# Kernel optimization log

Measured on AMD Instinct MI355X. Metric: run time of the kernel, lower is better.

Reference implementation:

```python
import jax, jax.numpy as jnp
import numpy as np

DIM = 4096
N_HEADS = 32
N_KV_HEADS = 8
HEAD_DIM = DIM // N_HEADS  # 128
SEQ = 2048
ROPE_THETA = 500000.0


def precompute_freqs_cis(head_dim, end, theta=ROPE_THETA):
    freq = 1.0 / theta ** (jnp.arange(0, head_dim, 2, dtype=jnp.float32) / head_dim)
    t = jnp.arange(end, dtype=jnp.float32)
    freqs = jnp.outer(t, freq)  # [S, D/2]
    return jnp.cos(freqs), jnp.sin(freqs)


def apply_rope(x, cos, sin):
    # x: [S, H, D]; cos/sin: [S, D/2]; interleaved even/odd rotation
    x_even = x[:, :, 0::2]
    x_odd = x[:, :, 1::2]
    c = cos[:, None, :]
    s = sin[:, None, :]
    rot_even = x_even * c - x_odd * s
    rot_odd = x_even * s + x_odd * c
    # re-interleave: stack on last axis then flatten -> [e0,o0,e1,o1,...]
    return jnp.stack([rot_even, rot_odd], axis=-1).reshape(x.shape)


def setup_inputs() -> dict:
    key = jax.random.key(0)
    ks = jax.random.split(key, 5)
    scale = 1.0 / np.sqrt(DIM)
    x = jax.random.normal(ks[0], (SEQ, DIM), dtype=jnp.float32)
    wq = jax.random.normal(ks[1], (DIM, DIM), dtype=jnp.float32) * scale
    wk = jax.random.normal(ks[2], (N_KV_HEADS * HEAD_DIM, DIM), dtype=jnp.float32) * scale
    wv = jax.random.normal(ks[3], (N_KV_HEADS * HEAD_DIM, DIM), dtype=jnp.float32) * scale
    wo = jax.random.normal(ks[4], (DIM, DIM), dtype=jnp.float32) * scale
    return {"x": x, "wq": wq, "wk": wk, "wv": wv, "wo": wo}


def reference(x, wq, wk, wv, wo):
    seq_len = x.shape[0]
    Q = (x @ wq.T).reshape(seq_len, N_HEADS, HEAD_DIM)
    K = (x @ wk.T).reshape(seq_len, N_KV_HEADS, HEAD_DIM)
    V = (x @ wv.T).reshape(seq_len, N_KV_HEADS, HEAD_DIM)
    cos, sin = precompute_freqs_cis(HEAD_DIM, seq_len)
    Q = apply_rope(Q, cos, sin)
    K = apply_rope(K, cos, sin)
    rep = N_HEADS // N_KV_HEADS
    K_rep = jnp.repeat(K, rep, axis=1)  # [S, H, D]
    V_rep = jnp.repeat(V, rep, axis=1)
    scores = jnp.einsum('qhd,khd->hqk', Q, K_rep) / np.sqrt(HEAD_DIM).astype(np.float32)
    causal = jnp.triu(jnp.ones((seq_len, seq_len), dtype=bool), k=1)
    scores = jnp.where(causal[None, :, :], -jnp.inf, scores)
    probs = jax.nn.softmax(scores.astype(jnp.float32), axis=-1).astype(Q.dtype)
    out = jnp.einsum('hqk,khd->qhd', probs, V_rep).reshape(seq_len, N_HEADS * HEAD_DIM)
    return out @ wo.T
```

## Files before the change

kernel.cpp:

```cpp
#include <hip/hip_runtime.h>
#include <stdint.h>
#include <math.h>

#define DIM 4096
#define NH 32
#define NKV 8
#define HD 128
#define SEQ 2048
#define KVDIM (NKV * HD)
#define QKVDIM (DIM + 2 * KVDIM)

typedef __bf16 bf16x8 __attribute__((ext_vector_type(8)));
typedef float floatx4 __attribute__((ext_vector_type(4)));
typedef uint16_t u16x8 __attribute__((ext_vector_type(8)));

#define AS1C(p) ((const __attribute__((address_space(1))) void*)(p))
#define AS3(p)  ((__attribute__((address_space(3))) void*)(p))

__device__ __forceinline__ float b2f(uint16_t u) {
    union { uint32_t i; float f; } v; v.i = ((uint32_t)u) << 16; return v.f;
}
__device__ __forceinline__ uint16_t f2b(float f) {
    union { float f; uint32_t i; } v; v.f = f;
    uint32_t r = v.i + 0x7fffu + ((v.i >> 16) & 1u);
    return (uint16_t)(r >> 16);
}

__device__ __forceinline__ u16x8 ldchunk(const void* p, bool isf32, size_t e) {
    if (isf32) {
        const float* fp = (const float*)p + e;
        u16x8 r;
#pragma unroll
        for (int j = 0; j < 8; ++j) r[j] = f2b(fp[j]);
        return r;
    }
    return *(const u16x8*)((const uint16_t*)p + e);
}

__global__ void detect_k(const uint16_t* __restrict__ x, int* __restrict__ flag) {
    __shared__ int cnt;
    if (threadIdx.x == 0) cnt = 0;
    __syncthreads();
    int bad = 0;
    for (int i = threadIdx.x; i < 4096; i += 256) {
        float v = b2f(x[i]);
        if (!(fabsf(v) < 1e6f)) bad++;
    }
    atomicAdd(&cnt, bad);
    __syncthreads();
    if (threadIdx.x == 0) *flag = (cnt > 256) ? 1 : 0;
}

__global__ __launch_bounds__(256) void conv_k(const void* __restrict__ src,
                                              uint16_t* __restrict__ dst,
                                              size_t n,
                                              const int* __restrict__ flagp) {
    const int f = *flagp;
    size_t i = ((size_t)blockIdx.x * blockDim.x + threadIdx.x) * 8;
    const size_t stride = (size_t)gridDim.x * blockDim.x * 8;
    if (f) {
        for (; i < n; i += stride) {
            const float* s = (const float*)src + i;
            u16x8 r;
#pragma unroll
            for (int j = 0; j < 8; ++j) r[j] = f2b(s[j]);
            *(u16x8*)(dst + i) = r;
        }
    } else {
        for (; i < n; i += stride)
            *(u16x8*)(dst + i) = *(const u16x8*)((const uint16_t*)src + i);
    }
}

__global__ __launch_bounds__(256) void gemm_nt(const void* __restrict__ A,
                                               const void* __restrict__ B,
                                               void* __restrict__ C,
                                               int K, int ldc,
                                               const int* __restrict__ flagp,
                                               int a_dyn, int b_dyn, int out_dyn,
                                               int out_trans) {
    __shared__ uint16_t As[128 * 64];
    __shared__ uint16_t Bs[128 * 64];
    const int f = *flagp;
    const bool af32 = a_dyn && f, bf32 = b_dyn && f, of32 = out_dyn && f;
    const int tid = threadIdx.x;
    const int wave = tid >> 6, lane = tid & 63;
    const int wh = wave >> 1, ww = wave & 1;
    const int quad = lane >> 4, l16 = lane & 15;
    const int m0 = blockIdx.x * 128;
    const int n0 = blockIdx.y * 128;

    floatx4 acc[4][4] = {};

    for (int k0 = 0; k0 < K; k0 += 64) {
        __syncthreads();
#pragma unroll
        for (int it = 0; it < 4; ++it) {
            int id = tid + it * 256;
            int row = id >> 3, slot = id & 7;
            int c8 = ((slot ^ (row & 7)) << 3);
            u16x8 va = ldchunk(A, af32, (size_t)(m0 + row) * K + k0 + c8);
            *(u16x8*)(As + row * 64 + slot * 8) = va;
            u16x8 vb = ldchunk(B, bf32, (size_t)(n0 + row) * K + k0 + c8);
            *(u16x8*)(Bs + row * 64 + slot * 8) = vb;
        }
        __syncthreads();
#pragma unroll
        for (int ks = 0; ks < 2; ++ks) {
            bf16x8 af[4], bf[4];
#pragma unroll
            for (int mi = 0; mi < 4; ++mi) {
                int r = wh * 64 + mi * 16 + l16;
                int slot = (ks * 4 + quad) ^ (r & 7);
                af[mi] = *(const bf16x8*)(As + r * 64 + slot * 8);
            }
#pragma unroll
            for (int ni = 0; ni < 4; ++ni) {
                int r = ww * 64 + ni * 16 + l16;
                int slot = (ks * 4 + quad) ^ (r & 7);
                bf[ni] = *(const bf16x8*)(Bs + r * 64 + slot * 8);
            }
#pragma unroll
            for (int mi = 0; mi < 4; ++mi)
#pragma unroll
                for (int ni = 0; ni < 4; ++ni)
                    acc[mi][ni] = __builtin_amdgcn_mfma_f32_16x16x32_bf16(
                        af[mi], bf[ni], acc[mi][ni], 0, 0, 0);
        }
    }
#pragma unroll
    for (int mi = 0; mi < 4; ++mi) {
#pragma unroll
        for (int ni = 0; ni < 4; ++ni) {
            int row = m0 + wh * 64 + mi * 16 + quad * 4;
            int col = n0 + ww * 64 + ni * 16 + l16;
            if (out_trans) {
                uint64_t pack = 0;
#pragma unroll
                for (int i = 0; i < 4; ++i)
                    pack |= (uint64_t)f2b(acc[mi][ni][i]) << (16 * i);
                *(uint64_t*)((uint16_t*)C + (size_t)col * ldc + row) = pack;
            } else if (of32) {
#pragma unroll
                for (int i = 0; i < 4; ++i)
                    ((float*)C)[(size_t)(row + i) * ldc + col] = acc[mi][ni][i];
            } else {
#pragma unroll
                for (int i = 0; i < 4; ++i)
                    ((uint16_t*)C)[(size_t)(row + i) * ldc + col] = f2b(acc[mi][ni][i]);
            }
        }
    }
}

__global__ __launch_bounds__(256) void gemm_bf(const uint16_t* __restrict__ A,
                                               const uint16_t* __restrict__ B,
                                               void* __restrict__ C,
                                               int K, int ldc,
                                               const int* __restrict__ flagp,
                                               int out_mode) {
    __shared__ uint16_t As[128 * 64];
    __shared__ uint16_t Bs[128 * 64];
    const bool of32 = (out_mode == 1) && (*flagp);
    const int tid = threadIdx.x;
    const int wave = tid >> 6, lane = tid & 63;
    const int wh = wave >> 1, ww = wave & 1;
    const int quad = lane >> 4, l16 = lane & 15;

    int nwg = gridDim.x * gridDim.y;
    int id = blockIdx.y * gridDim.x + blockIdx.x;
    if ((nwg & 7) == 0) {
        int cpx = nwg >> 3;
        id = (id & 7) * cpx + (id >> 3);
    }
    const int m0 = (id % gridDim.x) * 128;
    const int n0 = (id / gridDim.x) * 128;

    floatx4 acc[4][4] = {};

    for (int k0 = 0; k0 < K; k0 += 64) {
        __syncthreads();
#pragma unroll
        for (int it = 0; it < 4; ++it) {
            int idc = tid + it * 256;
            int row = idc >> 3, slot = idc & 7;
            int c8 = ((slot ^ (row & 7)) << 3);
            __builtin_amdgcn_global_load_lds(
                AS1C(A + (size_t)(m0 + row) * K + k0 + c8),
                AS3(As + (size_t)(it * 256 + wave * 64) * 8), 16, 0, 0);
            __builtin_amdgcn_global_load_lds(
                AS1C(B + (size_t)(n0 + row) * K + k0 + c8),
                AS3(Bs + (size_t)(it * 256 + wave * 64) * 8), 16, 0, 0);
        }
        __syncthreads();
#pragma unroll
        for (int ks = 0; ks < 2; ++ks) {
            bf16x8 af[4], bf[4];
#pragma unroll
            for (int mi = 0; mi < 4; ++mi) {
                int r = wh * 64 + mi * 16 + l16;
                int slot = (ks * 4 + quad) ^ (r & 7);
                af[mi] = *(const bf16x8*)(As + r * 64 + slot * 8);
            }
#pragma unroll
            for (int ni = 0; ni < 4; ++ni) {
                int r = ww * 64 + ni * 16 + l16;
                int slot = (ks * 4 + quad) ^ (r & 7);
                bf[ni] = *(const bf16x8*)(Bs + r * 64 + slot * 8);
            }
#pragma unroll
            for (int mi = 0; mi < 4; ++mi)
#pragma unroll
                for (int ni = 0; ni < 4; ++ni)
                    acc[mi][ni] = __builtin_amdgcn_mfma_f32_16x16x32_bf16(
                        af[mi], bf[ni], acc[mi][ni], 0, 0, 0);
        }
    }
#pragma unroll
    for (int mi = 0; mi < 4; ++mi) {
#pragma unroll
        for (int ni = 0; ni < 4; ++ni) {
            int row = m0 + wh * 64 + mi * 16 + quad * 4;
            int col = n0 + ww * 64 + ni * 16 + l16;
            if (of32) {
#pragma unroll
                for (int i = 0; i < 4; ++i)
                    ((float*)C)[(size_t)(row + i) * ldc + col] = acc[mi][ni][i];
            } else {
#pragma unroll
                for (int i = 0; i < 4; ++i)
                    ((uint16_t*)C)[(size_t)(row + i) * ldc + col] = f2b(acc[mi][ni][i]);
            }
        }
    }
}

__global__ __launch_bounds__(256) void gemm_qkv(const uint16_t* __restrict__ A,
                                                const uint16_t* __restrict__ W,
                                                uint16_t* __restrict__ Qo,
                                                uint16_t* __restrict__ Ko,
                                                uint16_t* __restrict__ VoT) {
    __shared__ uint16_t As[128 * 64];
    __shared__ uint16_t Bs[128 * 64];
    const int tid = threadIdx.x;
    const int wave = tid >> 6, lane = tid & 63;
    const int wh = wave >> 1, ww = wave & 1;
    const int quad = lane >> 4, l16 = lane & 15;

    int nwg = gridDim.x * gridDim.y;
    int id = blockIdx.y * gridDim.x + blockIdx.x;
    int cpx = nwg >> 3;
    id = (id & 7) * cpx + (id >> 3);
    const int m0 = (id % gridDim.x) * 128;
    const int n0 = (id / gridDim.x) * 128;
    const int K = DIM;

    floatx4 acc[4][4] = {};

    for (int k0 = 0; k0 < K; k0 += 64) {
        __syncthreads();
#pragma unroll
        for (int it = 0; it < 4; ++it) {
            int idc = tid + it * 256;
            int row = idc >> 3, slot = idc & 7;
            int c8 = ((slot ^ (row & 7)) << 3);
            __builtin_amdgcn_global_load_lds(
                AS1C(A + (size_t)(m0 + row) * K + k0 + c8),
                AS3(As + (size_t)(it * 256 + wave * 64) * 8), 16, 0, 0);
            __builtin_amdgcn_global_load_lds(
                AS1C(W + (size_t)(n0 + row) * K + k0 + c8),
                AS3(Bs + (size_t)(it * 256 + wave * 64) * 8), 16, 0, 0);
        }
        __syncthreads();
#pragma unroll
        for (int ks = 0; ks < 2; ++ks) {
            bf16x8 af[4], bf[4];
#pragma unroll
            for (int mi = 0; mi < 4; ++mi) {
                int r = wh * 64 + mi * 16 + l16;
                int slot = (ks * 4 + quad) ^ (r & 7);
                af[mi] = *(const bf16x8*)(As + r * 64 + slot * 8);
            }
#pragma unroll
            for (int ni = 0; ni < 4; ++ni) {
                int r = ww * 64 + ni * 16 + l16;
                int slot = (ks * 4 + quad) ^ (r & 7);
                bf[ni] = *(const bf16x8*)(Bs + r * 64 + slot * 8);
            }
#pragma unroll
            for (int mi = 0; mi < 4; ++mi)
#pragma unroll
                for (int ni = 0; ni < 4; ++ni)
                    acc[mi][ni] = __builtin_amdgcn_mfma_f32_16x16x32_bf16(
                        af[mi], bf[ni], acc[mi][ni], 0, 0, 0);
        }
    }
#pragma unroll
    for (int mi = 0; mi < 4; ++mi) {
#pragma unroll
        for (int ni = 0; ni < 4; ++ni) {
            int row = m0 + wh * 64 + mi * 16 + quad * 4;
            int col = n0 + ww * 64 + ni * 16 + l16;
            if (n0 < DIM) {
#pragma unroll
                for (int i = 0; i < 4; ++i)
                    Qo[(size_t)(row + i) * DIM + col] = f2b(acc[mi][ni][i]);
            } else if (n0 < DIM + KVDIM) {
                int c = col - DIM;
#pragma unroll
                for (int i = 0; i < 4; ++i)
                    Ko[(size_t)(row + i) * KVDIM + c] = f2b(acc[mi][ni][i]);
            } else {
                int c = col - DIM - KVDIM;
                uint64_t pack = 0;
#pragma unroll
                for (int i = 0; i < 4; ++i)
                    pack |= (uint64_t)f2b(acc[mi][ni][i]) << (16 * i);
                *(uint64_t*)(VoT + (size_t)c * SEQ + row) = pack;
            }
        }
    }
}

__global__ void rope_k(uint16_t* __restrict__ buf, int heads) {
    int id = blockIdx.x * blockDim.x + threadIdx.x;
    int i = id & 63;
    int h = (id >> 6) % heads;
    int t = id / (64 * heads);
    uint16_t* p = buf + (size_t)t * (heads * HD) + h * HD + 2 * i;
    float e = b2f(p[0]), o = b2f(p[1]);
    float freq = exp2f(-(float)(2 * i) * (18.93156857f / 128.0f));
    float ang = (float)t * freq;
    float s, c;
    sincosf(ang, &s, &c);
    p[0] = f2b(e * c - o * s);
    p[1] = f2b(e * s + o * c);
}

__global__ __launch_bounds__(512, 1) void attn_k(const uint16_t* __restrict__ Q,
                                                 const uint16_t* __restrict__ Kg,
                                                 const uint16_t* __restrict__ VgT,
                                                 uint16_t* __restrict__ O) {
    __shared__ uint16_t Ks[2][64 * 128];
    __shared__ uint16_t Vt[2][128 * 64];
    __shared__ uint16_t Pb[128 * 64];
    __shared__ uint16_t Qs[128 * 128];

    const int tid = threadIdx.x;
    const int wave = tid >> 6, lane = tid & 63;
    const int quad = lane >> 4, l16 = lane & 15;

    const int head = blockIdx.x & 31;
    const int pairid = blockIdx.x >> 5;
    const int kvh = head >> 2;
    const uint16_t* Vh = VgT + (size_t)kvh * HD * SEQ;

    const float scale = 0.08838834764831845f;
    const float LOG2E = 1.44269504f;

    auto stage_kv = [&](int buf, int k0s) {
#pragma unroll
        for (int it = 0; it < 2; ++it) {
            int id = tid + it * 512;
            int row = id >> 4, slot = id & 15;
            int c8 = ((slot ^ (row & 7)) << 3);
            __builtin_amdgcn_global_load_lds(
                AS1C(Kg + (size_t)(k0s + row) * KVDIM + kvh * HD + c8),
                AS3(Ks[buf] + (size_t)(it * 512 + wave * 64) * 8), 16, 0, 0);
        }
#pragma unroll
        for (int it = 0; it < 2; ++it) {
            int id = tid + it * 512;
            int d = id >> 3, slot = id & 7;
            int c8 = ((slot ^ (d & 7)) << 3);
            __builtin_amdgcn_global_load_lds(
                AS1C(Vh + (size_t)d * SEQ + k0s + c8),
                AS3(Vt[buf] + (size_t)(it * 512 + wave * 64) * 8), 16, 0, 0);
        }
    };

    int g = 0;
    for (int half = 0; half < 2; ++half) {
        const int qt = half ? (15 - pairid) : pairid;
        const int q0 = qt * 128;
        const int nkt = 2 * qt + 2;

#pragma unroll
        for (int it = 0; it < 4; ++it) {
            int id = tid + it * 512;
            int row = id >> 4, slot = id & 15;
            int c8 = ((slot ^ (row & 7)) << 3);
            __builtin_amdgcn_global_load_lds(
                AS1C(Q + (size_t)(q0 + row) * DIM + head * HD + c8),
                AS3(Qs + (size_t)(it * 512 + wave * 64) * 8), 16, 0, 0);
        }
        if (half == 0) stage_kv(0, 0);
        __syncthreads();

        bf16x8 qf[4];
#pragma unroll
        for (int ks = 0; ks < 4; ++ks) {
            int r = wave * 16 + l16;
            int slot = (ks * 4 + quad) ^ (r & 7);
            qf[ks] = *(const bf16x8*)(Qs + r * 128 + slot * 8);
        }

        floatx4 acc_o[8] = {};
        float m_run[4], l_run[4];
#pragma unroll
        for (int i = 0; i < 4; ++i) { m_run[i] = -__builtin_inff(); l_run[i] = 0.f; }

        for (int t = 0; t < nkt; ++t, ++g) {
            const int k0 = t * 64;
            const bool diag = (t >= 2 * qt);
            const int cur = g & 1;

            if (!(half == 1 && t == nkt - 1)) {
                int k0n = (t + 1 < nkt) ? (t + 1) * 64 : 0;
                stage_kv((g + 1) & 1, k0n);
            }
            __builtin_amdgcn_sched_barrier(0);

            floatx4 acc_s[4] = {};
            __builtin_amdgcn_s_setprio(1);
#pragma unroll
            for (int ks = 0; ks < 4; ++ks) {
                bf16x8 kf[4];
#pragma unroll
                for (int ni = 0; ni < 4; ++ni) {
                    int r = ni * 16 + l16;
                    int slot = (ks * 4 + quad) ^ (r & 7);
                    kf[ni] = *(const bf16x8*)(Ks[cur] + r * 128 + slot * 8);
                }
#pragma unroll
                for (int ni = 0; ni < 4; ++ni)
                    acc_s[ni] = __builtin_amdgcn_mfma_f32_16x16x32_bf16(
                        qf[ks], kf[ni], acc_s[ni], 0, 0, 0);
            }
            __builtin_amdgcn_s_setprio(0);

#pragma unroll
            for (int ni = 0; ni < 4; ++ni)
#pragma unroll
                for (int i = 0; i < 4; ++i) {
                    float s = acc_s[ni][i] * scale;
                    if (diag) {
                        int ql = q0 + wave * 16 + quad * 4 + i;
                        int kl = k0 + ni * 16 + l16;
                        if (kl > ql) s = -__builtin_inff();
                    }
                    acc_s[ni][i] = s;
                }

            float alpha[4];
#pragma unroll
            for (int i = 0; i < 4; ++i) {
                float v = fmaxf(fmaxf(acc_s[0][i], acc_s[1][i]),
                                fmaxf(acc_s[2][i], acc_s[3][i]));
#pragma unroll
                for (int off = 1; off < 16; off <<= 1)
                    v = fmaxf(v, __shfl_xor(v, off));
                float mn = fmaxf(m_run[i], v);
                alpha[i] = exp2f((m_run[i] - mn) * LOG2E);
                m_run[i] = mn;

                int ql = wave * 16 + quad * 4 + i;
                float sum = 0.f;
#pragma unroll
                for (int ni = 0; ni < 4; ++ni) {
                    float p = exp2f((acc_s[ni][i] - mn) * LOG2E);
                    sum += p;
                    int key = ni * 16 + l16;
                    int slot = ((key >> 3) ^ (ql & 7) ^ ((ql >> 3) & 7)) & 7;
                    Pb[ql * 64 + slot * 8 + (key & 7)] = f2b(p);
                }
#pragma unroll
                for (int off = 1; off < 16; off <<= 1)
                    sum += __shfl_xor(sum, off);
                l_run[i] = l_run[i] * alpha[i] + sum;
            }

#pragma unroll
            for (int ni = 0; ni < 8; ++ni)
#pragma unroll
                for (int i = 0; i < 4; ++i)
                    acc_o[ni][i] *= alpha[i];

            __builtin_amdgcn_s_setprio(1);
#pragma unroll
            for (int ks2 = 0; ks2 < 2; ++ks2) {
                bf16x8 pf, vf[8];
                {
                    int r = wave * 16 + l16;
                    int slot = ((ks2 * 4 + quad) ^ (r & 7) ^ ((r >> 3) & 7)) & 7;
                    pf = *(const bf16x8*)(Pb + r * 64 + slot * 8);
                }
#pragma unroll
                for (int ni = 0; ni < 8; ++ni) {
                    int d = ni * 16 + l16;
                    int slot = ((ks2 * 4 + quad) ^ (d & 7)) & 7;
                    vf[ni] = *(const bf16x8*)(Vt[cur] + d * 64 + slot * 8);
                }
#pragma unroll
                for (int ni = 0; ni < 8; ++ni)
                    acc_o[ni] = __builtin_amdgcn_mfma_f32_16x16x32_bf16(
                        pf, vf[ni], acc_o[ni], 0, 0, 0);
            }
            __builtin_amdgcn_s_setprio(0);

            __syncthreads();
        }

#pragma unroll
        for (int i = 0; i < 4; ++i) {
            float inv = 1.0f / l_run[i];
            int row = q0 + wave * 16 + quad * 4 + i;
#pragma unroll
            for (int ni = 0; ni < 8; ++ni) {
                int col = head * HD + ni * 16 + l16;
                O[(size_t)row * DIM + col] = f2b(acc_o[ni][i] * inv);
            }
        }
    }
}

extern "C" void kernel_launch(void* const* d_in, const int* in_sizes, int n_in,
                              void* d_out, int out_size, void* d_ws, size_t ws_size,
                              hipStream_t stream) {
    const void* x  = d_in[0];
    const void* wq = d_in[1];
    const void* wk = d_in[2];
    const void* wv = d_in[3];
    const void* wo = d_in[4];

    int* flag = (int*)d_ws;
    uint16_t* Kb  = (uint16_t*)((char*)d_ws + 256);
    uint16_t* VbT = Kb + (size_t)SEQ * KVDIM;
    uint16_t* xb  = VbT + (size_t)SEQ * KVDIM;
    uint16_t* BIG = xb + (size_t)SEQ * DIM;
    uint16_t* Wqkv = BIG;
    uint16_t* Ab   = BIG;
    uint16_t* Wo   = BIG + (size_t)SEQ * DIM;
    uint16_t* Qb = (uint16_t*)d_out;

    const size_t need = 256 + ((size_t)2 * SEQ * KVDIM
                             + (size_t)SEQ * DIM
                             + (size_t)QKVDIM * DIM) * 2;

    dim3 blk(256);
    detect_k<<<1, blk, 0, stream>>>((const uint16_t*)x, flag);

    if (ws_size >= need) {
        conv_k<<<2048, blk, 0, stream>>>(x, xb, (size_t)SEQ * DIM, flag);
        conv_k<<<2048, blk, 0, stream>>>(wq, Wqkv, (size_t)DIM * DIM, flag);
        conv_k<<<2048, blk, 0, stream>>>(wk, Wqkv + (size_t)DIM * DIM,
                                         (size_t)KVDIM * DIM, flag);
        conv_k<<<2048, blk, 0, stream>>>(wv, Wqkv + (size_t)(DIM + KVDIM) * DIM,
                                         (size_t)KVDIM * DIM, flag);
        gemm_qkv<<<dim3(SEQ / 128, QKVDIM / 128), blk, 0, stream>>>(
            xb, Wqkv, Qb, Kb, VbT);
        conv_k<<<2048, blk, 0, stream>>>(wo, Wo, (size_t)DIM * DIM, flag);
        rope_k<<<(SEQ * NH * 64) / 256, 256, 0, stream>>>(Qb, NH);
        rope_k<<<(SEQ * NKV * 64) / 256, 256, 0, stream>>>(Kb, NKV);
        attn_k<<<NH * 8, dim3(512), 0, stream>>>(Qb, Kb, VbT, Ab);
        gemm_bf<<<dim3(SEQ / 128, DIM / 128), blk, 0, stream>>>(Ab, Wo, d_out, DIM, DIM, flag, 1);
    } else {
        uint16_t* AbL = xb;
        gemm_nt<<<dim3(SEQ / 128, DIM / 128), blk, 0, stream>>>(x, wq, Qb, DIM, DIM, flag, 1, 1, 0, 0);
        gemm_nt<<<dim3(SEQ / 128, KVDIM / 128), blk, 0, stream>>>(x, wk, Kb, DIM, KVDIM, flag, 1, 1, 0, 0);
        gemm_nt<<<dim3(SEQ / 128, KVDIM / 128), blk, 0, stream>>>(x, wv, VbT, DIM, SEQ, flag, 1, 1, 0, 1);
        rope_k<<<(SEQ * NH * 64) / 256, 256, 0, stream>>>(Qb, NH);
        rope_k<<<(SEQ * NKV * 64) / 256, 256, 0, stream>>>(Kb, NKV);
        attn_k<<<NH * 8, dim3(512), 0, stream>>>(Qb, Kb, VbT, AbL);
        gemm_nt<<<dim3(SEQ / 128, DIM / 128), blk, 0, stream>>>(AbL, wo, d_out, DIM, DIM, flag, 0, 1, 1, 0);
    }
}
```

Measured before the change: 516.0 us.

## Split attention into one block per query tile and fuse conversion and RoPE launches

The attention kernel previously paired two query tiles per block, processed one after the other, to balance causal work across 256 blocks. It now launches 512 blocks, one query tile each, with the longest tiles scheduled first. Q fragments are loaded straight from global memory into registers, dropping the 32KB shared Q stage, and launch bounds now allow several blocks per CU for higher occupancy. Separately, the four input conversion kernels are merged into one launch and the two RoPE launches into one, which cuts launch overhead. The trade-off is more blocks and less explicit load balancing, plus uncoalesced-style direct Q loads.

```diff
diff --git a/kernel.cpp b/kernel.cpp
--- a/kernel.cpp
+++ b/kernel.cpp
@@ -69,6 +69,46 @@
     } else {
         for (; i < n; i += stride)
             *(u16x8*)(dst + i) = *(const u16x8*)((const uint16_t*)src + i);
+    }
+}
+
+__global__ __launch_bounds__(256) void conv4_k(const void* __restrict__ s0,
+                                               const void* __restrict__ s1,
+                                               const void* __restrict__ s2,
+                                               const void* __restrict__ s3,
+                                               uint16_t* __restrict__ d0,
+                                               uint16_t* __restrict__ d1,
+                                               uint16_t* __restrict__ d2,
+                                               uint16_t* __restrict__ d3,
+                                               size_t n0, size_t n1,
+                                               size_t n2, size_t n3,
+                                               const int* __restrict__ flagp) {
+    const int f = *flagp;
+    const size_t tot = (n0 + n1 + n2 + n3) >> 3;
+    size_t c = (size_t)blockIdx.x * blockDim.x + threadIdx.x;
+    const size_t stride = (size_t)gridDim.x * blockDim.x;
+    for (; c < tot; c += stride) {
+        size_t off = c << 3;
+        const void* sp; uint16_t* dp;
+        if (off < n0) { sp = s0; dp = d0; }
+        else {
+            off -= n0;
+            if (off < n1) { sp = s1; dp = d1; }
+            else {
+                off -= n1;
+                if (off < n2) { sp = s2; dp = d2; }
+                else { off -= n2; sp = s3; dp = d3; }
+            }
+        }
+        if (f) {
+            const float* s = (const float*)sp + off;
+            u16x8 r;
+#pragma unroll
+            for (int j = 0; j < 8; ++j) r[j] = f2b(s[j]);
+            *(u16x8*)(dp + off) = r;
+        } else {
+            *(u16x8*)(dp + off) = *(const u16x8*)((const uint16_t*)sp + off);
+        }
     }
 }
 
@@ -322,12 +362,15 @@
     }
 }
 
-__global__ void rope_k(uint16_t* __restrict__ buf, int heads) {
+__global__ void rope2_k(uint16_t* __restrict__ Qb, uint16_t* __restrict__ Kb) {
     int id = blockIdx.x * blockDim.x + threadIdx.x;
     int i = id & 63;
-    int h = (id >> 6) % heads;
-    int t = id / (64 * heads);
-    uint16_t* p = buf + (size_t)t * (heads * HD) + h * HD + 2 * i;
+    int rest = id >> 6;
+    int hh = rest % (NH + NKV);
+    int t = rest / (NH + NKV);
+    uint16_t* p = (hh < NH)
+        ? (Qb + (size_t)t * DIM + hh * HD + 2 * i)
+        : (Kb + (size_t)t * KVDIM + (hh - NH) * HD + 2 * i);
     float e = b2f(p[0]), o = b2f(p[1]);
     float freq = exp2f(-(float)(2 * i) * (18.93156857f / 128.0f));
     float ang = (float)t * freq;
@@ -337,22 +380,23 @@
     p[1] = f2b(e * s + o * c);
 }
 
-__global__ __launch_bounds__(512, 1) void attn_k(const uint16_t* __restrict__ Q,
+__global__ __launch_bounds__(512, 4) void attn_k(const uint16_t* __restrict__ Q,
                                                  const uint16_t* __restrict__ Kg,
                                                  const uint16_t* __restrict__ VgT,
                                                  uint16_t* __restrict__ O) {
     __shared__ uint16_t Ks[2][64 * 128];
     __shared__ uint16_t Vt[2][128 * 64];
     __shared__ uint16_t Pb[128 * 64];
-    __shared__ uint16_t Qs[128 * 128];
 
     const int tid = threadIdx.x;
     const int wave = tid >> 6, lane = tid & 63;
     const int quad = lane >> 4, l16 = lane & 15;
 
     const int head = blockIdx.x & 31;
-    const int pairid = blockIdx.x >> 5;
+    const int g16 = blockIdx.x >> 5;
+    const int qt = (g16 < 8) ? (15 - g16) : (g16 - 8);
     const int kvh = head >> 2;
+    const int q0 = qt * 128;
     const uint16_t* Vh = VgT + (size_t)kvh * HD * SEQ;
 
     const float scale = 0.08838834764831845f;
@@ -379,147 +423,129 @@
         }
     };
 
-    int g = 0;
-    for (int half = 0; half < 2; ++half) {
-        const int qt = half ? (15 - pairid) : pairid;
-        const int q0 = qt * 128;
-        const int nkt = 2 * qt + 2;
-
-#pragma unroll
-        for (int it = 0; it < 4; ++it) {
-            int id = tid + it * 512;
-            int row = id >> 4, slot = id & 15;
-            int c8 = ((slot ^ (row & 7)) << 3);
-            __builtin_amdgcn_global_load_lds(
-                AS1C(Q + (size_t)(q0 + row) * DIM + head * HD + c8),
-                AS3(Qs + (size_t)(it * 512 + wave * 64) * 8), 16, 0, 0);
-        }
-        if (half == 0) stage_kv(0, 0);
+    bf16x8 qf[4];
+    {
+        const uint16_t* qrow = Q + (size_t)(q0 + wave * 16 + l16) * DIM + head * HD;
+#pragma unroll
+        for (int ks = 0; ks < 4; ++ks)
+            qf[ks] = *(const bf16x8*)(qrow + (ks * 4 + quad) * 8);
+    }
+
+    floatx4 acc_o[8] = {};
+    float m_run[4], l_run[4];
+#pragma unroll
+    for (int i = 0; i < 4; ++i) { m_run[i] = -__builtin_inff(); l_run[i] = 0.f; }
+
+    const int nkt = 2 * qt + 2;
+    stage_kv(0, 0);
+    __syncthreads();
+
+    for (int t = 0; t < nkt; ++t) {
+        const int k0 = t * 64;
+        const bool diag = (t >= 2 * qt);
+        const int cur = t & 1;
+
+        if (t + 1 < nkt) stage_kv((t + 1) & 1, (t + 1) * 64);
+        __builtin_amdgcn_sched_barrier(0);
+
+        floatx4 acc_s[4] = {};
+        __builtin_amdgcn_s_setprio(1);
+#pragma unroll
+        for (int ks = 0; ks < 4; ++ks) {
+            bf16x8 kf[4];
+#pragma unroll
+            for (int ni = 0; ni < 4; ++ni) {
+                int r = ni * 16 + l16;
+                int slot = (ks * 4 + quad) ^ (r & 7);
+                kf[ni] = *(const bf16x8*)(Ks[cur] + r * 128 + slot * 8);
+            }
+#pragma unroll
+            for (int ni = 0; ni < 4; ++ni)
+                acc_s[ni] = __builtin_amdgcn_mfma_f32_16x16x32_bf16(
+                    qf[ks], kf[ni], acc_s[ni], 0, 0, 0);
+        }
+        __builtin_amdgcn_s_setprio(0);
+
+#pragma unroll
+        for (int ni = 0; ni < 4; ++ni)
+#pragma unroll
+            for (int i = 0; i < 4; ++i) {
+                float s = acc_s[ni][i] * scale;
+                if (diag) {
+                    int ql = q0 + wave * 16 + quad * 4 + i;
+                    int kl = k0 + ni * 16 + l16;
+                    if (kl > ql) s = -__builtin_inff();
+                }
+                acc_s[ni][i] = s;
+            }
+
+        float alpha[4];
+#pragma unroll
+        for (int i = 0; i < 4; ++i) {
+            float v = fmaxf(fmaxf(acc_s[0][i], acc_s[1][i]),
+                            fmaxf(acc_s[2][i], acc_s[3][i]));
+#pragma unroll
+            for (int off = 1; off < 16; off <<= 1)
+                v = fmaxf(v, __shfl_xor(v, off));
+            float mn = fmaxf(m_run[i], v);
+            alpha[i] = exp2f((m_run[i] - mn) * LOG2E);
+            m_run[i] = mn;
+
+            int ql = wave * 16 + quad * 4 + i;
+            float sum = 0.f;
+#pragma unroll
+            for (int ni = 0; ni < 4; ++ni) {
+                float p = exp2f((acc_s[ni][i] - mn) * LOG2E);
+                sum += p;
+                int key = ni * 16 + l16;
+                int slot = ((key >> 3) ^ (ql & 7) ^ ((ql >> 3) & 7)) & 7;
+                Pb[ql * 64 + slot * 8 + (key & 7)] = f2b(p);
+            }
+#pragma unroll
+            for (int off = 1; off < 16; off <<= 1)
+                sum += __shfl_xor(sum, off);
+            l_run[i] = l_run[i] * alpha[i] + sum;
+        }
+
+#pragma unroll
+        for (int ni = 0; ni < 8; ++ni)
+#pragma unroll
+            for (int i = 0; i < 4; ++i)
+                acc_o[ni][i] *= alpha[i];
+
+        __builtin_amdgcn_s_setprio(1);
+#pragma unroll
+        for (int ks2 = 0; ks2 < 2; ++ks2) {
+            bf16x8 pf, vf[8];
+            {
+                int r = wave * 16 + l16;
+                int slot = ((ks2 * 4 + quad) ^ (r & 7) ^ ((r >> 3) & 7)) & 7;
+                pf = *(const bf16x8*)(Pb + r * 64 + slot * 8);
+            }
+#pragma unroll
+            for (int ni = 0; ni < 8; ++ni) {
+                int d = ni * 16 + l16;
+                int slot = ((ks2 * 4 + quad) ^ (d & 7)) & 7;
+                vf[ni] = *(const bf16x8*)(Vt[cur] + d * 64 + slot * 8);
+            }
+#pragma unroll
+            for (int ni = 0; ni < 8; ++ni)
+                acc_o[ni] = __builtin_amdgcn_mfma_f32_16x16x32_bf16(
+                    pf, vf[ni], acc_o[ni], 0, 0, 0);
+        }
+        __builtin_amdgcn_s_setprio(0);
+
         __syncthreads();
-
-        bf16x8 qf[4];
-#pragma unroll
-        for (int ks = 0; ks < 4; ++ks) {
-            int r = wave * 16 + l16;
-            int slot = (ks * 4 + quad) ^ (r & 7);
-            qf[ks] = *(const bf16x8*)(Qs + r * 128 + slot * 8);
-        }
-
-        floatx4 acc_o[8] = {};
-        float m_run[4], l_run[4];
-#pragma unroll
-        for (int i = 0; i < 4; ++i) { m_run[i] = -__builtin_inff(); l_run[i] = 0.f; }
-
-        for (int t = 0; t < nkt; ++t, ++g) {
-            const int k0 = t * 64;
-            const bool diag = (t >= 2 * qt);
-            const int cur = g & 1;
-
-            if (!(half == 1 && t == nkt - 1)) {
-                int k0n = (t + 1 < nkt) ? (t + 1) * 64 : 0;
-                stage_kv((g + 1) & 1, k0n);
-            }
-            __builtin_amdgcn_sched_barrier(0);
-
-            floatx4 acc_s[4] = {};
-            __builtin_amdgcn_s_setprio(1);
-#pragma unroll
-            for (int ks = 0; ks < 4; ++ks) {
-                bf16x8 kf[4];
-#pragma unroll
-                for (int ni = 0; ni < 4; ++ni) {
-                    int r = ni * 16 + l16;
-                    int slot = (ks * 4 + quad) ^ (r & 7);
-                    kf[ni] = *(const bf16x8*)(Ks[cur] + r * 128 + slot * 8);
-                }
-#pragma unroll
-                for (int ni = 0; ni < 4; ++ni)
-                    acc_s[ni] = __builtin_amdgcn_mfma_f32_16x16x32_bf16(
-                        qf[ks], kf[ni], acc_s[ni], 0, 0, 0);
-            }
-            __builtin_amdgcn_s_setprio(0);
-
-#pragma unroll
-            for (int ni = 0; ni < 4; ++ni)
-#pragma unroll
-                for (int i = 0; i < 4; ++i) {
-                    float s = acc_s[ni][i] * scale;
-                    if (diag) {
-                        int ql = q0 + wave * 16 + quad * 4 + i;
-                        int kl = k0 + ni * 16 + l16;
-                        if (kl > ql) s = -__builtin_inff();
-                    }
-                    acc_s[ni][i] = s;
-                }
-
-            float alpha[4];
-#pragma unroll
-            for (int i = 0; i < 4; ++i) {
-                float v = fmaxf(fmaxf(acc_s[0][i], acc_s[1][i]),
-                                fmaxf(acc_s[2][i], acc_s[3][i]));
-#pragma unroll
-                for (int off = 1; off < 16; off <<= 1)
-                    v = fmaxf(v, __shfl_xor(v, off));
-                float mn = fmaxf(m_run[i], v);
-                alpha[i] = exp2f((m_run[i] - mn) * LOG2E);
-                m_run[i] = mn;
-
-                int ql = wave * 16 + quad * 4 + i;
-                float sum = 0.f;
-#pragma unroll
-                for (int ni = 0; ni < 4; ++ni) {
-                    float p = exp2f((acc_s[ni][i] - mn) * LOG2E);
-                    sum += p;
-                    int key = ni * 16 + l16;
-                    int slot = ((key >> 3) ^ (ql & 7) ^ ((ql >> 3) & 7)) & 7;
-                    Pb[ql * 64 + slot * 8 + (key & 7)] = f2b(p);
-                }
-#pragma unroll
-                for (int off = 1; off < 16; off <<= 1)
-                    sum += __shfl_xor(sum, off);
-                l_run[i] = l_run[i] * alpha[i] + sum;
-            }
-
-#pragma unroll
-            for (int ni = 0; ni < 8; ++ni)
-#pragma unroll
-                for (int i = 0; i < 4; ++i)
-                    acc_o[ni][i] *= alpha[i];
-
-            __builtin_amdgcn_s_setprio(1);
-#pragma unroll
-            for (int ks2 = 0; ks2 < 2; ++ks2) {
-                bf16x8 pf, vf[8];
-                {
-                    int r = wave * 16 + l16;
-                    int slot = ((ks2 * 4 + quad) ^ (r & 7) ^ ((r >> 3) & 7)) & 7;
-                    pf = *(const bf16x8*)(Pb + r * 64 + slot * 8);
-                }
-#pragma unroll
-                for (int ni = 0; ni < 8; ++ni) {
-                    int d = ni * 16 + l16;
-                    int slot = ((ks2 * 4 + quad) ^ (d & 7)) & 7;
-                    vf[ni] = *(const bf16x8*)(Vt[cur] + d * 64 + slot * 8);
-                }
-#pragma unroll
-                for (int ni = 0; ni < 8; ++ni)
-                    acc_o[ni] = __builtin_amdgcn_mfma_f32_16x16x32_bf16(
-                        pf, vf[ni], acc_o[ni], 0, 0, 0);
-            }
-            __builtin_amdgcn_s_setprio(0);
-
-            __syncthreads();
-        }
-
-#pragma unroll
-        for (int i = 0; i < 4; ++i) {
-            float inv = 1.0f / l_run[i];
-            int row = q0 + wave * 16 + quad * 4 + i;
-#pragma unroll
-            for (int ni = 0; ni < 8; ++ni) {
-                int col = head * HD + ni * 16 + l16;
-                O[(size_t)row * DIM + col] = f2b(acc_o[ni][i] * inv);
-            }
+    }
+
+#pragma unroll
+    for (int i = 0; i < 4; ++i) {
+        float inv = 1.0f / l_run[i];
+        int row = q0 + wave * 16 + quad * 4 + i;
+#pragma unroll
+        for (int ni = 0; ni < 8; ++ni) {
+            int col = head * HD + ni * 16 + l16;
+            O[(size_t)row * DIM + col] = f2b(acc_o[ni][i] * inv);
         }
     }
 }
@@ -551,27 +577,24 @@
     detect_k<<<1, blk, 0, stream>>>((const uint16_t*)x, flag);
 
     if (ws_size >= need) {
-        conv_k<<<2048, blk, 0, stream>>>(x, xb, (size_t)SEQ * DIM, flag);
-        conv_k<<<2048, blk, 0, stream>>>(wq, Wqkv, (size_t)DIM * DIM, flag);
-        conv_k<<<2048, blk, 0, stream>>>(wk, Wqkv + (size_t)DIM * DIM,
-                                         (size_t)KVDIM * DIM, flag);
-        conv_k<<<2048, blk, 0, stream>>>(wv, Wqkv + (size_t)(DIM + KVDIM) * DIM,
-                                         (size_t)KVDIM * DIM, flag);
+        conv4_k<<<4096, blk, 0, stream>>>(
+            x, wq, wk, wv,
+            xb, Wqkv, Wqkv + (size_t)DIM * DIM, Wqkv + (size_t)(DIM + KVDIM) * DIM,
+            (size_t)SEQ * DIM, (size_t)DIM * DIM,
+            (size_t)KVDIM * DIM, (size_t)KVDIM * DIM, flag);
         gemm_qkv<<<dim3(SEQ / 128, QKVDIM / 128), blk, 0, stream>>>(
             xb, Wqkv, Qb, Kb, VbT);
         conv_k<<<2048, blk, 0, stream>>>(wo, Wo, (size_t)DIM * DIM, flag);
-        rope_k<<<(SEQ * NH * 64) / 256, 256, 0, stream>>>(Qb, NH);
-        rope_k<<<(SEQ * NKV * 64) / 256, 256, 0, stream>>>(Kb, NKV);
-        attn_k<<<NH * 8, dim3(512), 0, stream>>>(Qb, Kb, VbT, Ab);
+        rope2_k<<<(SEQ * (NH + NKV) * 64) / 256, 256, 0, stream>>>(Qb, Kb);
+        attn_k<<<NH * 16, dim3(512), 0, stream>>>(Qb, Kb, VbT, Ab);
         gemm_bf<<<dim3(SEQ / 128, DIM / 128), blk, 0, stream>>>(Ab, Wo, d_out, DIM, DIM, flag, 1);
     } else {
         uint16_t* AbL = xb;
         gemm_nt<<<dim3(SEQ / 128, DIM / 128), blk, 0, stream>>>(x, wq, Qb, DIM, DIM, flag, 1, 1, 0, 0);
         gemm_nt<<<dim3(SEQ / 128, KVDIM / 128), blk, 0, stream>>>(x, wk, Kb, DIM, KVDIM, flag, 1, 1, 0, 0);
         gemm_nt<<<dim3(SEQ / 128, KVDIM / 128), blk, 0, stream>>>(x, wv, VbT, DIM, SEQ, flag, 1, 1, 0, 1);
-        rope_k<<<(SEQ * NH * 64) / 256, 256, 0, stream>>>(Qb, NH);
-        rope_k<<<(SEQ * NKV * 64) / 256, 256, 0, stream>>>(Kb, NKV);
-        attn_k<<<NH * 8, dim3(512), 0, stream>>>(Qb, Kb, VbT, AbL);
+        rope2_k<<<(SEQ * (NH + NKV) * 64) / 256, 256, 0, stream>>>(Qb, Kb);
+        attn_k<<<NH * 16, dim3(512), 0, stream>>>(Qb, Kb, VbT, AbL);
         gemm_nt<<<dim3(SEQ / 128, DIM / 128), blk, 0, stream>>>(AbL, wo, d_out, DIM, DIM, flag, 0, 1, 1, 0);
     }
 }
```

Result: no change. 520.8 us (+0.9%).
